# Optimization experiments

Hardware: AMD Instinct MI355X
Metric: run time of the kernel (lower is better)

The kernel has to match this reference:

```python
import jax, jax.numpy as jnp
import numpy as np

NUM_PERS = 16
D = 128
N = 4096
EPSILON = 0.1
EPS_NORM = 1e-12  # matches torch F.normalize default eps


def setup_inputs() -> dict:
    key = jax.random.key(0)
    k1, k2 = jax.random.split(key)
    context = jax.random.normal(k1, (N, D), dtype=jnp.float32)
    # xavier_uniform for shape (num_pers, input_size): bound = sqrt(6/(fan_in+fan_out))
    bound = float(np.sqrt(6.0 / (NUM_PERS + D)))
    weight_tensor = jax.random.uniform(k2, (NUM_PERS, D), dtype=jnp.float32,
                                       minval=-bound, maxval=bound)
    return {"context": context, "weight_tensor": weight_tensor}


def reference(context, weight_tensor):
    # context: [N, D]; weight_tensor: [P, D]
    # per-perspective weighted features: [P, N, D]
    context_fc = context[None, :, :] * weight_tensor[:, None, :]
    # L2 normalize along feature dim (torch F.normalize: x / max(||x||, eps))
    norm = jnp.maximum(jnp.linalg.norm(context_fc, axis=-1, keepdims=True), EPS_NORM)
    context_norm = context_fc / norm
    # cosine similarity per perspective, mean over perspectives: [N, N]
    attention = jnp.einsum('pnd,pmd->pnm', context_norm, context_norm).mean(0)
    # epsilon neighbourhood with markoff_value = 0
    mask = (attention > EPSILON).astype(attention.dtype)
    return attention * mask
```

## Files before the change

### kernel.cpp

```cpp
#include <hip/hip_runtime.h>
#include <math.h>

#define N 4096
#define D 128
#define P 16
#define KK 2048
#define NT 32
#define NBLK (NT * (NT + 1) / 2)
#define LCAP 2048
#define CAP (1u << 20)
#define WIN 1.5e-3f
#define ZSCALE 256.0f
#define OSCALE (1.0f / 16777216.0f * 16.0f)

typedef _Float16 half_t;
typedef __attribute__((ext_vector_type(8))) _Float16 f16x8;
typedef __attribute__((ext_vector_type(4))) float f32x4;
typedef __attribute__((address_space(1))) const unsigned int* gptr_t;
typedef __attribute__((address_space(3))) unsigned int* lptr_t;

__global__ __launch_bounds__(256) void k_pack(const float* __restrict__ c,
                                              const float* __restrict__ w,
                                              double* __restrict__ rnorm,
                                              half_t* __restrict__ zb,
                                              unsigned* gcnt, unsigned* govf,
                                              int do_init) {
    int n = blockIdx.x, tid = threadIdx.x;
    if (do_init && n == 0 && tid == 0) { *gcnt = 0; *govf = 0; }
    int p = tid >> 4, d0 = (tid & 15) * 8;
    const float* cc = c + (size_t)n * D + d0;
    const float* ww = w + (size_t)p * D + d0;
    float cv[8], wv[8];
    *(float4*)&cv[0] = *(const float4*)&cc[0];
    *(float4*)&cv[4] = *(const float4*)&cc[4];
    *(float4*)&wv[0] = *(const float4*)&ww[0];
    *(float4*)&wv[4] = *(const float4*)&ww[4];
    double s = 0.0;
#pragma unroll
    for (int i = 0; i < 8; ++i) {
        double v = (double)cv[i] * (double)wv[i];
        s += v * v;
    }
#pragma unroll
    for (int o = 1; o < 16; o <<= 1) s += __shfl_xor(s, o, 64);
    double rn = 1.0 / fmax(sqrt(s), 1e-12);
    if ((tid & 15) == 0) rnorm[p * N + n] = rn;
    float rnf = (float)rn;
    f16x8 o8;
#pragma unroll
    for (int i = 0; i < 8; ++i) o8[i] = (half_t)(cv[i] * wv[i] * rnf * ZSCALE);
    *(f16x8*)&zb[(size_t)n * KK + tid * 8] = o8;
}

template <bool FUSED>
__global__ __launch_bounds__(256, 4) void k_gemm(const half_t* __restrict__ zb,
                                                 float* __restrict__ out,
                                                 unsigned* __restrict__ gcnt,
                                                 unsigned* __restrict__ govf,
                                                 unsigned* __restrict__ glist) {
    __shared__ __align__(16) half_t As[2][128 * 32];
    __shared__ __align__(16) half_t Bs[2][128 * 32];
    __shared__ unsigned lds_list[LCAP];
    __shared__ unsigned lds_cnt, lds_base, lds_tot;

    int tid = threadIdx.x;
    if (FUSED && tid == 0) lds_cnt = 0;

    int lane = tid & 63, wv = tid >> 6;
    int wr = wv >> 1, wc = wv & 1;

    int braw = blockIdx.x;
    int b = (braw & 7) * (NBLK / 8) + (braw >> 3);
    int ti = 0;
    while (b >= NT - ti) { b -= NT - ti; ++ti; }
    int tj = ti + b;
    int n0 = ti * 128, m0 = tj * 128;

    f32x4 acc[4][4] = {};
    int lrow = lane >> 2;
    int lchunk = (((lane & 3) ^ ((lrow >> 1) & 3)) * 8);

    auto STAGE = [&](int buf, int k0) {
#pragma unroll
        for (int h = 0; h < 2; ++h) {
            int s = h * 4 + wv;
            int row = s * 16 + lrow;
            __builtin_amdgcn_global_load_lds(
                (gptr_t)(zb + (size_t)(n0 + row) * KK + k0 + lchunk),
                (lptr_t)(&As[buf][s * 512]), 16, 0, 0);
            __builtin_amdgcn_global_load_lds(
                (gptr_t)(zb + (size_t)(m0 + row) * KK + k0 + lchunk),
                (lptr_t)(&Bs[buf][s * 512]), 16, 0, 0);
        }
    };

    int kk_c = lane >> 4;
    int rsel = lane & 15;
    int kphys = (kk_c ^ ((rsel >> 1) & 3)) * 8;

    auto COMPUTE = [&](int cur) {
        f16x8 af[4], bfr[4];
#pragma unroll
        for (int f = 0; f < 4; ++f) {
            af[f]  = *(f16x8*)&As[cur][(wr * 64 + f * 16 + rsel) * 32 + kphys];
            bfr[f] = *(f16x8*)&Bs[cur][(wc * 64 + f * 16 + rsel) * 32 + kphys];
        }
#pragma unroll
        for (int i = 0; i < 4; ++i)
#pragma unroll
            for (int j = 0; j < 4; ++j)
                acc[i][j] = __builtin_amdgcn_mfma_f32_16x16x32_f16(af[i], bfr[j], acc[i][j], 0, 0, 0);
    };

    STAGE(0, 0);

#pragma unroll 2
    for (int t = 0; t < 63; ++t) {
        int cur = t & 1;
        STAGE(cur ^ 1, (t + 1) * 32);
        asm volatile("s_waitcnt vmcnt(4)" ::: "memory");
        __builtin_amdgcn_sched_barrier(0);
        __builtin_amdgcn_s_barrier();
        __builtin_amdgcn_sched_barrier(0);
        COMPUTE(cur);
        asm volatile("s_waitcnt lgkmcnt(0)" ::: "memory");
        __builtin_amdgcn_sched_barrier(0);
        __builtin_amdgcn_s_barrier();
        __builtin_amdgcn_sched_barrier(0);
    }
    asm volatile("s_waitcnt vmcnt(0)" ::: "memory");
    __builtin_amdgcn_sched_barrier(0);
    __builtin_amdgcn_s_barrier();
    __builtin_amdgcn_sched_barrier(0);
    COMPUTE(1);

    int colD = lane & 15, rq = lane >> 4;
    bool mir = (ti != tj);
#pragma unroll
    for (int i = 0; i < 4; ++i)
#pragma unroll
        for (int j = 0; j < 4; ++j) {
            int rbase = n0 + wr * 64 + i * 16 + rq * 4;
            int ccol = m0 + wc * 64 + j * 16 + colD;
            float4 mv;
#pragma unroll
            for (int q = 0; q < 4; ++q) {
                float a = acc[i][j][q] * OSCALE;
                float sv;
                if (FUSED) {
                    bool flg = fabsf(a - 0.1f) < WIN;
                    sv = flg ? a : (a > 0.1f ? a : 0.0f);
                    if (flg) {
                        unsigned pos = atomicAdd(&lds_cnt, 1u);
                        unsigned ent = (unsigned)(rbase + q) | ((unsigned)ccol << 12) |
                                       (mir ? (1u << 24) : 0u);
                        if (pos < LCAP) lds_list[pos] = ent;
                    }
                } else {
                    sv = a;
                }
                out[(size_t)(rbase + q) * N + ccol] = sv;
                ((float*)&mv)[q] = sv;
            }
            if (mir) *(float4*)&out[(size_t)ccol * N + rbase] = mv;
        }

    if (FUSED) {
        __syncthreads();
        if (tid == 0) {
            unsigned tot = lds_cnt;
            unsigned cnt = tot > LCAP ? LCAP : tot;
            lds_tot = cnt;
            lds_base = atomicAdd(gcnt, cnt);
            if (tot > LCAP) atomicOr(govf, 1u);
        }
        __syncthreads();
        unsigned cnt = lds_tot, base = lds_base;
        for (unsigned e = tid; e < cnt; e += 256) {
            unsigned gi = base + e;
            if (gi < CAP) glist[gi] = lds_list[e];
            else atomicOr(govf, 1u);
        }
    }
}

__global__ __launch_bounds__(256) void k_fix2(const float* __restrict__ c,
                                              const float* __restrict__ w,
                                              const double* __restrict__ rnorm,
                                              const unsigned* __restrict__ gcnt,
                                              const unsigned* __restrict__ glist,
                                              float* __restrict__ out) {
    __shared__ double w2[D * P];
    for (int e = threadIdx.x; e < P * D; e += 256) {
        int p = e >> 7, d = e & 127;
        double wv = (double)w[p * D + d];
        w2[d * P + p] = wv * wv;
    }
    __syncthreads();

    unsigned count = *gcnt;
    if (count > CAP) count = CAP;
    unsigned stride = gridDim.x * 256;
    for (unsigned e = blockIdx.x * 256 + threadIdx.x; e < count; e += stride) {
        unsigned u = glist[e];
        int n = u & 4095, m = (u >> 12) & 4095;
        const float* cn = c + (size_t)n * D;
        const float* cm = c + (size_t)m * D;
        double acc[P];
#pragma unroll
        for (int p = 0; p < P; ++p) acc[p] = 0.0;
        for (int d0 = 0; d0 < D; d0 += 4) {
            float4 a4 = *(const float4*)&cn[d0];
            float4 b4 = *(const float4*)&cm[d0];
            float av[4] = {a4.x, a4.y, a4.z, a4.w};
            float bv[4] = {b4.x, b4.y, b4.z, b4.w};
#pragma unroll
            for (int q = 0; q < 4; ++q) {
                double pr = (double)av[q] * (double)bv[q];
#pragma unroll
                for (int p = 0; p < P; ++p) acc[p] += pr * w2[(d0 + q) * P + p];
            }
        }
        double t = 0.0;
#pragma unroll
        for (int p = 0; p < P; ++p)
            t += acc[p] * (rnorm[p * N + n] * rnorm[p * N + m]);
        double fin = t * 0.0625;
        float res = (fin > 0.1) ? (float)fin : 0.0f;
        out[(size_t)n * N + m] = res;
        if (u >> 24) out[(size_t)m * N + n] = res;
    }
}

__global__ __launch_bounds__(256) void k_guard(const float* __restrict__ c,
                                               const float* __restrict__ w,
                                               const double* __restrict__ rnorm,
                                               const unsigned* __restrict__ govf,
                                               float* __restrict__ out) {
    if (*govf == 0) return;
    __shared__ double w2[D * P];
    for (int e = threadIdx.x; e < P * D; e += 256) {
        int p = e >> 7, d = e & 127;
        double wv = (double)w[p * D + d];
        w2[d * P + p] = wv * wv;
    }
    __syncthreads();
    size_t stride = (size_t)gridDim.x * 256;
    for (size_t idx = (size_t)blockIdx.x * 256 + threadIdx.x; idx < (size_t)N * N;
         idx += stride) {
        float a = out[idx];
        if (fabsf(a - 0.1f) >= WIN) {
            out[idx] = (a > 0.1f) ? a : 0.0f;
            continue;
        }
        int n = (int)(idx >> 12), m = (int)(idx & (N - 1));
        const float* cn = c + (size_t)n * D;
        const float* cm = c + (size_t)m * D;
        double acc[P];
#pragma unroll
        for (int p = 0; p < P; ++p) acc[p] = 0.0;
        for (int d0 = 0; d0 < D; d0 += 4) {
            float4 a4 = *(const float4*)&cn[d0];
            float4 b4 = *(const float4*)&cm[d0];
            float av[4] = {a4.x, a4.y, a4.z, a4.w};
            float bv[4] = {b4.x, b4.y, b4.z, b4.w};
#pragma unroll
            for (int q = 0; q < 4; ++q) {
                double pr = (double)av[q] * (double)bv[q];
#pragma unroll
                for (int p = 0; p < P; ++p) acc[p] += pr * w2[(d0 + q) * P + p];
            }
        }
        double t = 0.0;
#pragma unroll
        for (int p = 0; p < P; ++p)
            t += acc[p] * (rnorm[p * N + n] * rnorm[p * N + m]);
        double fin = t * 0.0625;
        out[idx] = (fin > 0.1) ? (float)fin : 0.0f;
    }
}

__global__ __launch_bounds__(256) void k_fix_full(const float* __restrict__ c,
                                                  const float* __restrict__ w,
                                                  const double* __restrict__ rnorm,
                                                  float* __restrict__ out) {
    __shared__ double w2[D * P];
    for (int e = threadIdx.x; e < P * D; e += 256) {
        int p = e >> 7, d = e & 127;
        double wv = (double)w[p * D + d];
        w2[d * P + p] = wv * wv;
    }
    __syncthreads();
    size_t stride = (size_t)gridDim.x * 256;
    for (size_t idx = (size_t)blockIdx.x * 256 + threadIdx.x; idx < (size_t)N * N;
         idx += stride) {
        float a = out[idx];
        if (fabsf(a - 0.1f) >= WIN) {
            out[idx] = (a > 0.1f) ? a : 0.0f;
            continue;
        }
        int n = (int)(idx >> 12), m = (int)(idx & (N - 1));
        const float* cn = c + (size_t)n * D;
        const float* cm = c + (size_t)m * D;
        double acc[P];
#pragma unroll
        for (int p = 0; p < P; ++p) acc[p] = 0.0;
        for (int d0 = 0; d0 < D; d0 += 4) {
            float4 a4 = *(const float4*)&cn[d0];
            float4 b4 = *(const float4*)&cm[d0];
            float av[4] = {a4.x, a4.y, a4.z, a4.w};
            float bv[4] = {b4.x, b4.y, b4.z, b4.w};
#pragma unroll
            for (int q = 0; q < 4; ++q) {
                double pr = (double)av[q] * (double)bv[q];
#pragma unroll
                for (int p = 0; p < P; ++p) acc[p] += pr * w2[(d0 + q) * P + p];
            }
        }
        double t = 0.0;
#pragma unroll
        for (int p = 0; p < P; ++p)
            t += acc[p] * (rnorm[p * N + n] * rnorm[p * N + m]);
        double fin = t * 0.0625;
        out[idx] = (fin > 0.1) ? (float)fin : 0.0f;
    }
}

extern "C" void kernel_launch(void* const* d_in, const int* in_sizes, int n_in,
                              void* d_out, int out_size, void* d_ws, size_t ws_size,
                              hipStream_t stream) {
    const float* c = (const float*)d_in[0];
    const float* w = (const float*)d_in[1];
    float* out = (float*)d_out;
    char* ws = (char*)d_ws;

    double* rnorm = (double*)ws;
    size_t off = (size_t)P * N * 8;
    unsigned* gcnt = (unsigned*)(ws + off);
    unsigned* govf = gcnt + 1;
    unsigned* glist = (unsigned*)(ws + off + 128);
    half_t* zb = (half_t*)(ws + off + 128 + (size_t)CAP * 4);
    size_t need = off + 128 + (size_t)CAP * 4 + (size_t)N * KK * 2;

    if (ws_size >= need) {
        k_pack<<<N, 256, 0, stream>>>(c, w, rnorm, zb, gcnt, govf, 1);
        k_gemm<true><<<NBLK, 256, 0, stream>>>(zb, out, gcnt, govf, glist);
        k_fix2<<<1024, 256, 0, stream>>>(c, w, rnorm, gcnt, glist, out);
        k_guard<<<1024, 256, 0, stream>>>(c, w, rnorm, govf, out);
    } else {
        half_t* zb2 = (half_t*)(ws + off);
        k_pack<<<N, 256, 0, stream>>>(c, w, rnorm, zb2, nullptr, nullptr, 0);
        k_gemm<false><<<NBLK, 256, 0, stream>>>(zb2, out, nullptr, nullptr, nullptr);
        k_fix_full<<<4096, 256, 0, stream>>>(c, w, rnorm, out);
    }
}
```

Baseline: 97.75 us.

## Use full 256x256 GEMM tiles with 512 threads instead of symmetric 128 tiles

Replaces the upper-triangular 128x128 tiling, which mirrored its results, with a full grid of 256x256 tiles computed by 8 waves, each holding a 128x64 accumulator. This removes the strided transposed mirror stores and raises arithmetic intensity per loaded tile, but it recomputes the symmetric half, doubling MFMA work. It also reuses the staging LDS for the candidate list (larger capacity, no mirror flag) and adds s_setprio around the MFMA bursts. The larger accumulator footprint raises register pressure and leaves only 256 blocks for the GPU.

```diff
diff --git a/kernel.cpp b/kernel.cpp
--- a/kernel.cpp
+++ b/kernel.cpp
@@ -5,9 +5,9 @@
 #define D 128
 #define P 16
 #define KK 2048
-#define NT 32
-#define NBLK (NT * (NT + 1) / 2)
-#define LCAP 2048
+#define NTB 16
+#define NBLK (NTB * NTB)
+#define LCAPD 15000
 #define CAP (1u << 20)
 #define WIN 1.5e-3f
 #define ZSCALE 256.0f
@@ -53,130 +53,145 @@
 }
 
 template <bool FUSED>
-__global__ __launch_bounds__(256, 4) void k_gemm(const half_t* __restrict__ zb,
+__global__ __launch_bounds__(512, 2) void k_gemm(const half_t* __restrict__ zb,
                                                  float* __restrict__ out,
                                                  unsigned* __restrict__ gcnt,
                                                  unsigned* __restrict__ govf,
                                                  unsigned* __restrict__ glist) {
-    __shared__ __align__(16) half_t As[2][128 * 32];
-    __shared__ __align__(16) half_t Bs[2][128 * 32];
-    __shared__ unsigned lds_list[LCAP];
-    __shared__ unsigned lds_cnt, lds_base, lds_tot;
+    __shared__ __align__(16) half_t smbuf[2][16384];
+    __shared__ unsigned wl3[4];
 
     int tid = threadIdx.x;
-    if (FUSED && tid == 0) lds_cnt = 0;
-
-    int lane = tid & 63, wv = tid >> 6;
-    int wr = wv >> 1, wc = wv & 1;
+    int lane = tid & 63, wid = tid >> 6;
+    int wm = wid >> 2, wn = wid & 3;
 
     int braw = blockIdx.x;
-    int b = (braw & 7) * (NBLK / 8) + (braw >> 3);
-    int ti = 0;
-    while (b >= NT - ti) { b -= NT - ti; ++ti; }
-    int tj = ti + b;
-    int n0 = ti * 128, m0 = tj * 128;
-
-    f32x4 acc[4][4] = {};
-    int lrow = lane >> 2;
-    int lchunk = (((lane & 3) ^ ((lrow >> 1) & 3)) * 8);
-
-    auto STAGE = [&](int buf, int k0) {
-#pragma unroll
-        for (int h = 0; h < 2; ++h) {
-            int s = h * 4 + wv;
-            int row = s * 16 + lrow;
-            __builtin_amdgcn_global_load_lds(
-                (gptr_t)(zb + (size_t)(n0 + row) * KK + k0 + lchunk),
-                (lptr_t)(&As[buf][s * 512]), 16, 0, 0);
-            __builtin_amdgcn_global_load_lds(
-                (gptr_t)(zb + (size_t)(m0 + row) * KK + k0 + lchunk),
-                (lptr_t)(&Bs[buf][s * 512]), 16, 0, 0);
-        }
+    int b = (braw & 7) * 32 + (braw >> 3);
+    int bi = b >> 4, bj = b & 15;
+    int n0 = bi * 256, m0 = bj * 256;
+
+    int rsel = lane & 15, kk_c = lane >> 4;
+    int pc8 = (kk_c ^ ((rsel >> 1) & 3)) * 8;
+
+    int srow = tid >> 2;
+    int schunk8 = ((tid & 3) ^ ((tid >> 3) & 3)) * 8;
+
+    f32x4 acc[8][4] = {};
+
+    auto STAGE = [&](int p, int kt) {
+        int k0 = kt * 32;
+        half_t* A = &smbuf[p][0];
+        half_t* B = &smbuf[p][8192];
+        __builtin_amdgcn_global_load_lds(
+            (gptr_t)(zb + (size_t)(n0 + srow) * KK + k0 + schunk8),
+            (lptr_t)(A + tid * 8), 16, 0, 0);
+        __builtin_amdgcn_global_load_lds(
+            (gptr_t)(zb + (size_t)(n0 + 128 + srow) * KK + k0 + schunk8),
+            (lptr_t)(A + 4096 + tid * 8), 16, 0, 0);
+        __builtin_amdgcn_global_load_lds(
+            (gptr_t)(zb + (size_t)(m0 + srow) * KK + k0 + schunk8),
+            (lptr_t)(B + tid * 8), 16, 0, 0);
+        __builtin_amdgcn_global_load_lds(
+            (gptr_t)(zb + (size_t)(m0 + 128 + srow) * KK + k0 + schunk8),
+            (lptr_t)(B + 4096 + tid * 8), 16, 0, 0);
     };
 
-    int kk_c = lane >> 4;
-    int rsel = lane & 15;
-    int kphys = (kk_c ^ ((rsel >> 1) & 3)) * 8;
-
-    auto COMPUTE = [&](int cur) {
-        f16x8 af[4], bfr[4];
-#pragma unroll
-        for (int f = 0; f < 4; ++f) {
-            af[f]  = *(f16x8*)&As[cur][(wr * 64 + f * 16 + rsel) * 32 + kphys];
-            bfr[f] = *(f16x8*)&Bs[cur][(wc * 64 + f * 16 + rsel) * 32 + kphys];
-        }
-#pragma unroll
-        for (int i = 0; i < 4; ++i)
-#pragma unroll
-            for (int j = 0; j < 4; ++j)
-                acc[i][j] = __builtin_amdgcn_mfma_f32_16x16x32_f16(af[i], bfr[j], acc[i][j], 0, 0, 0);
-    };
-
     STAGE(0, 0);
+    asm volatile("s_waitcnt vmcnt(0)" ::: "memory");
+    __builtin_amdgcn_sched_barrier(0);
+    __builtin_amdgcn_s_barrier();
+    __builtin_amdgcn_sched_barrier(0);
 
 #pragma unroll 2
-    for (int t = 0; t < 63; ++t) {
-        int cur = t & 1;
-        STAGE(cur ^ 1, (t + 1) * 32);
-        asm volatile("s_waitcnt vmcnt(4)" ::: "memory");
+    for (int kt = 0; kt < 64; ++kt) {
+        int p = kt & 1;
+        if (kt < 63) {
+            STAGE(p ^ 1, kt + 1);
+            asm volatile("s_waitcnt vmcnt(4)" ::: "memory");
+        } else {
+            asm volatile("s_waitcnt vmcnt(0)" ::: "memory");
+        }
         __builtin_amdgcn_sched_barrier(0);
         __builtin_amdgcn_s_barrier();
         __builtin_amdgcn_sched_barrier(0);
-        COMPUTE(cur);
+
+        const half_t* A = &smbuf[p][0];
+        const half_t* B = &smbuf[p][8192];
+        f16x8 af[4], bfr[4];
+#pragma unroll
+        for (int fj = 0; fj < 4; ++fj)
+            bfr[fj] = *(const f16x8*)&B[(wn * 64 + fj * 16 + rsel) * 32 + pc8];
+#pragma unroll
+        for (int fi = 0; fi < 4; ++fi)
+            af[fi] = *(const f16x8*)&A[(wm * 128 + fi * 16 + rsel) * 32 + pc8];
+        __builtin_amdgcn_s_setprio(1);
+#pragma unroll
+        for (int fi = 0; fi < 4; ++fi)
+#pragma unroll
+            for (int fj = 0; fj < 4; ++fj)
+                acc[fi][fj] = __builtin_amdgcn_mfma_f32_16x16x32_f16(af[fi], bfr[fj], acc[fi][fj], 0, 0, 0);
+        __builtin_amdgcn_s_setprio(0);
+#pragma unroll
+        for (int fi = 0; fi < 4; ++fi)
+            af[fi] = *(const f16x8*)&A[(wm * 128 + 64 + fi * 16 + rsel) * 32 + pc8];
+        __builtin_amdgcn_s_setprio(1);
+#pragma unroll
+        for (int fi = 0; fi < 4; ++fi)
+#pragma unroll
+            for (int fj = 0; fj < 4; ++fj)
+                acc[4 + fi][fj] = __builtin_amdgcn_mfma_f32_16x16x32_f16(af[fi], bfr[fj], acc[4 + fi][fj], 0, 0, 0);
+        __builtin_amdgcn_s_setprio(0);
+
         asm volatile("s_waitcnt lgkmcnt(0)" ::: "memory");
         __builtin_amdgcn_sched_barrier(0);
         __builtin_amdgcn_s_barrier();
         __builtin_amdgcn_sched_barrier(0);
     }
-    asm volatile("s_waitcnt vmcnt(0)" ::: "memory");
-    __builtin_amdgcn_sched_barrier(0);
-    __builtin_amdgcn_s_barrier();
-    __builtin_amdgcn_sched_barrier(0);
-    COMPUTE(1);
-
-    int colD = lane & 15, rq = lane >> 4;
-    bool mir = (ti != tj);
-#pragma unroll
-    for (int i = 0; i < 4; ++i)
-#pragma unroll
-        for (int j = 0; j < 4; ++j) {
-            int rbase = n0 + wr * 64 + i * 16 + rq * 4;
-            int ccol = m0 + wc * 64 + j * 16 + colD;
-            float4 mv;
+
+    unsigned* lds_list = (unsigned*)&smbuf[0][0];
+    if (FUSED) {
+        if (tid == 0) wl3[0] = 0;
+        __syncthreads();
+    }
+
+    int colD = rsel, rq = kk_c;
+#pragma unroll
+    for (int fi = 0; fi < 8; ++fi)
+#pragma unroll
+        for (int fj = 0; fj < 4; ++fj) {
+            int rbase = n0 + wm * 128 + fi * 16 + rq * 4;
+            int ccol = m0 + wn * 64 + fj * 16 + colD;
 #pragma unroll
             for (int q = 0; q < 4; ++q) {
-                float a = acc[i][j][q] * OSCALE;
+                float a = acc[fi][fj][q] * OSCALE;
                 float sv;
                 if (FUSED) {
                     bool flg = fabsf(a - 0.1f) < WIN;
                     sv = flg ? a : (a > 0.1f ? a : 0.0f);
                     if (flg) {
-                        unsigned pos = atomicAdd(&lds_cnt, 1u);
-                        unsigned ent = (unsigned)(rbase + q) | ((unsigned)ccol << 12) |
-                                       (mir ? (1u << 24) : 0u);
-                        if (pos < LCAP) lds_list[pos] = ent;
+                        unsigned pos = atomicAdd(&wl3[0], 1u);
+                        if (pos < LCAPD)
+                            lds_list[pos] = (unsigned)(rbase + q) | ((unsigned)ccol << 12);
                     }
                 } else {
                     sv = a;
                 }
                 out[(size_t)(rbase + q) * N + ccol] = sv;
-                ((float*)&mv)[q] = sv;
             }
-            if (mir) *(float4*)&out[(size_t)ccol * N + rbase] = mv;
         }
 
     if (FUSED) {
         __syncthreads();
         if (tid == 0) {
-            unsigned tot = lds_cnt;
-            unsigned cnt = tot > LCAP ? LCAP : tot;
-            lds_tot = cnt;
-            lds_base = atomicAdd(gcnt, cnt);
-            if (tot > LCAP) atomicOr(govf, 1u);
+            unsigned tot = wl3[0];
+            unsigned cnt = tot > LCAPD ? LCAPD : tot;
+            wl3[2] = cnt;
+            wl3[1] = atomicAdd(gcnt, cnt);
+            if (tot > LCAPD) atomicOr(govf, 1u);
         }
         __syncthreads();
-        unsigned cnt = lds_tot, base = lds_base;
-        for (unsigned e = tid; e < cnt; e += 256) {
+        unsigned cnt = wl3[2], base = wl3[1];
+        for (unsigned e = tid; e < cnt; e += 512) {
             unsigned gi = base + e;
             if (gi < CAP) glist[gi] = lds_list[e];
             else atomicOr(govf, 1u);
@@ -344,13 +359,13 @@
 
     if (ws_size >= need) {
         k_pack<<<N, 256, 0, stream>>>(c, w, rnorm, zb, gcnt, govf, 1);
-        k_gemm<true><<<NBLK, 256, 0, stream>>>(zb, out, gcnt, govf, glist);
+        k_gemm<true><<<NBLK, 512, 0, stream>>>(zb, out, gcnt, govf, glist);
         k_fix2<<<1024, 256, 0, stream>>>(c, w, rnorm, gcnt, glist, out);
         k_guard<<<1024, 256, 0, stream>>>(c, w, rnorm, govf, out);
     } else {
         half_t* zb2 = (half_t*)(ws + off);
         k_pack<<<N, 256, 0, stream>>>(c, w, rnorm, zb2, nullptr, nullptr, 0);
-        k_gemm<false><<<NBLK, 256, 0, stream>>>(zb2, out, nullptr, nullptr, nullptr);
+        k_gemm<false><<<NBLK, 512, 0, stream>>>(zb2, out, nullptr, nullptr, nullptr);
         k_fix_full<<<4096, 256, 0, stream>>>(c, w, rnorm, out);
     }
 }
```

Measured after the change: 118.3 us. 21.0% more time.
